# Performance work log

Measured on AMD Instinct MI355X. Metric: run time of the kernel, lower is better.

The kernel has to match this reference:

```python
import jax, jax.numpy as jnp
import numpy as np

NEG_SLOPE = 0.2
LN_EPS = 1e-5


def _layernorm(x, g, b):
    mu = jnp.mean(x, axis=-1, keepdims=True)
    var = jnp.mean(jnp.square(x - mu), axis=-1, keepdims=True)
    return (x - mu) * jax.lax.rsqrt(var + LN_EPS) * g + b


def _gat_layer(x, src, dst, ew, W, al, ar, bias, resW, act):
    # x: [N, F_in], W: [F_in, H*D], al/ar: [H, D], bias: [H*D]
    N = x.shape[0]
    H, D = al.shape
    feat = (x @ W).reshape(N, H, D)
    el = jnp.einsum('nhd,hd->nh', feat, al)          # [N, H]
    er = jnp.einsum('nhd,hd->nh', feat, ar)          # [N, H]
    e = jax.nn.leaky_relu(el[src] + er[dst], NEG_SLOPE)  # [E, H]
    # segment softmax over incoming edges of each destination node
    emax = jax.ops.segment_max(e, dst, num_segments=N)
    emax = jnp.where(jnp.isfinite(emax), emax, 0.0)
    ex = jnp.exp(e - emax[dst])
    den = jax.ops.segment_sum(ex, dst, num_segments=N)
    a = ex / den[dst] * ew[:, None]                  # [E, H] (edge_weight scales post-softmax, DGL semantics)
    msg = feat[src] * a[:, :, None]                  # [E, H, D]
    rst = jax.ops.segment_sum(msg, dst, num_segments=N)  # [N, H, D]
    res = (x @ resW).reshape(N, H, D) if resW is not None else x.reshape(N, H, D)
    rst = rst + res + bias.reshape(1, H, D)
    if act is not None:
        rst = act(rst)
    return rst.reshape(N, H * D)


def setup_inputs() -> dict:
    key = jax.random.key(0)
    ks = jax.random.split(key, 24)
    N, E, F_in, H, D = 100000, 1600000, 256, 4, 32
    HD = H * D
    s = 0.1
    inp = {
        'x': jax.random.normal(ks[0], (N, F_in), jnp.float32),
        'src': jax.random.randint(ks[1], (E,), 0, N, jnp.int32),
        'dst': jax.random.randint(ks[2], (E,), 0, N, jnp.int32),
        'edge_weight': jax.random.uniform(ks[3], (E,), jnp.float32),
        # layer 0: in 256 -> 4 heads x 32, residual Linear
        'W0': jax.random.normal(ks[4], (F_in, HD), jnp.float32) * s,
        'al0': jax.random.normal(ks[5], (H, D), jnp.float32) * s,
        'ar0': jax.random.normal(ks[6], (H, D), jnp.float32) * s,
        'b0': jnp.zeros((HD,), jnp.float32),
        'resW0': jax.random.normal(ks[7], (F_in, HD), jnp.float32) * s,
        'ln0_g': jnp.ones((HD,), jnp.float32),
        'ln0_b': jnp.zeros((HD,), jnp.float32),
        # layer 1: 128 -> 4x32, identity residual
        'W1': jax.random.normal(ks[8], (HD, HD), jnp.float32) * s,
        'al1': jax.random.normal(ks[9], (H, D), jnp.float32) * s,
        'ar1': jax.random.normal(ks[10], (H, D), jnp.float32) * s,
        'b1': jnp.zeros((HD,), jnp.float32),
        'ln1_g': jnp.ones((HD,), jnp.float32),
        'ln1_b': jnp.zeros((HD,), jnp.float32),
        # layer 2 (last, no activation)
        'W2': jax.random.normal(ks[11], (HD, HD), jnp.float32) * s,
        'al2': jax.random.normal(ks[12], (H, D), jnp.float32) * s,
        'ar2': jax.random.normal(ks[13], (H, D), jnp.float32) * s,
        'b2': jnp.zeros((HD,), jnp.float32),
        'ln2_g': jnp.ones((HD,), jnp.float32),
        'ln2_b': jnp.zeros((HD,), jnp.float32),
    }
    return inp


def reference(x, src, dst, edge_weight,
              W0, al0, ar0, b0, resW0, ln0_g, ln0_b,
              W1, al1, ar1, b1, ln1_g, ln1_b,
              W2, al2, ar2, b2, ln2_g, ln2_b):
    h = _gat_layer(x, src, dst, edge_weight, W0, al0, ar0, b0, resW0, jax.nn.elu)
    h = _layernorm(h, ln0_g, ln0_b)
    h = _gat_layer(h, src, dst, edge_weight, W1, al1, ar1, b1, None, jax.nn.elu)
    h = _layernorm(h, ln1_g, ln1_b)
    h = _gat_layer(h, src, dst, edge_weight, W2, al2, ar2, b2, None, None)
    h = _layernorm(h, ln2_g, ln2_b)
    return h
```

## Files before the change

kernel.cpp:

```cpp
#include <hip/hip_runtime.h>
#include <hip/hip_bf16.h>
#include <hip/hip_fp16.h>
#include <math.h>

#define DEV __device__ __forceinline__

typedef short v8s __attribute__((ext_vector_type(8)));
typedef float v4f __attribute__((ext_vector_type(4)));
typedef __fp16 fp16x2 __attribute__((ext_vector_type(2)));

DEV float bf2f(unsigned short u) {
    union { unsigned int i; float f; } c; c.i = ((unsigned int)u) << 16; return c.f;
}
DEV unsigned short f2bf(float f) {
    union { float f; unsigned int u; } c; c.f = f;
    unsigned int u = c.u;
    unsigned int r = u + 0x7fffu + ((u >> 16) & 1u);
    return (unsigned short)(r >> 16);
}
DEV unsigned short f2h(float f) {
    union { _Float16 h; unsigned short u; } c; c.h = (_Float16)f; return c.u;
}
DEV float h2f(unsigned short u) {
    union { unsigned short u; _Float16 h; } c; c.u = u; return (float)c.h;
}
DEV unsigned int pkdup(float x) {
    union { fp16x2 h; unsigned int u; } c;
    c.h = __builtin_amdgcn_cvt_pkrtz(x, x);
    return c.u;
}
DEV __half2 bitcast_h2(unsigned int u) {
    union { unsigned int u; __half2 h; } c; c.u = u; return c.h;
}

#if __has_builtin(__builtin_amdgcn_exp2f)
DEV float fexp2(float x) { return __builtin_amdgcn_exp2f(x); }
#else
DEV float fexp2(float x) { float r; asm("v_exp_f32 %0, %1" : "=v"(r) : "v"(x)); return r; }
#endif
#if __has_builtin(__builtin_amdgcn_rcpf)
DEV float frcp(float x) { return __builtin_amdgcn_rcpf(x); }
#else
DEV float frcp(float x) { float r; asm("v_rcp_f32 %0, %1" : "=v"(r) : "v"(x)); return r; }
#endif
#if __has_builtin(__builtin_amdgcn_rsqf)
DEV float frsq(float x) { return __builtin_amdgcn_rsqf(x); }
#else
DEV float frsq(float x) { float r; asm("v_rsq_f32 %0, %1" : "=v"(r) : "v"(x)); return r; }
#endif
DEV unsigned int cvtpk_bf16(float lo, float hi) {
    unsigned int r;
    asm("v_cvt_pk_bf16_f32 %0, %1, %2" : "=v"(r) : "v"(lo), "v"(hi));
    return r;
}

__global__ void detect_kernel(const unsigned short* __restrict__ w, int* __restrict__ flag) {
    __shared__ int cnt;
    if (threadIdx.x == 0) cnt = 0;
    __syncthreads();
    int c = 0;
    for (int i = threadIdx.x; i < 2048; i += 256) {
        unsigned short u = w[i * 2];
        int e = (u >> 7) & 0xff;
        if (e >= 110 && e <= 132) c++;
    }
    atomicAdd(&cnt, c);
    __syncthreads();
    if (threadIdx.x == 0) *flag = (cnt > 1024) ? 1 : 0;
}


__global__ void zero_kernel(int* __restrict__ p, int n) {
    int i = blockIdx.x * 256 + threadIdx.x;
    if (i < n) p[i] = 0;
}

__global__ void degree_kernel(const int* __restrict__ dst, int* __restrict__ deg, int E) {
    int i = blockIdx.x * 256 + threadIdx.x;
    if (i < E) atomicAdd(&deg[dst[i]], 1);
}

__global__ __launch_bounds__(1024)
void pscan_kernel(const int* __restrict__ deg, int* __restrict__ rowptr,
                  int* __restrict__ bsum, int n) {
    __shared__ int wtot[16];
    const int tid  = threadIdx.x;
    const int lane = tid & 63;
    const int wid  = tid >> 6;
    const int i0 = blockIdx.x * 4096 + tid * 4;
    int v0 = (i0     < n) ? deg[i0]     : 0;
    int v1 = (i0 + 1 < n) ? deg[i0 + 1] : 0;
    int v2 = (i0 + 2 < n) ? deg[i0 + 2] : 0;
    int v3 = (i0 + 3 < n) ? deg[i0 + 3] : 0;
    int s = v0 + v1 + v2 + v3;
    int sc = s;
    #pragma unroll
    for (int d = 1; d < 64; d <<= 1) {
        int t = __shfl_up(sc, d);
        if (lane >= d) sc += t;
    }
    if (lane == 63) wtot[wid] = sc;
    __syncthreads();
    int woff = 0, tot = 0;
    #pragma unroll
    for (int w = 0; w < 16; ++w) {
        int t = wtot[w];
        if (w < wid) woff += t;
        tot += t;
    }
    int p = woff + (sc - s);
    if (i0     < n) rowptr[i0]     = p; p += v0;
    if (i0 + 1 < n) rowptr[i0 + 1] = p; p += v1;
    if (i0 + 2 < n) rowptr[i0 + 2] = p; p += v2;
    if (i0 + 3 < n) rowptr[i0 + 3] = p;
    if (tid == 0) bsum[blockIdx.x] = tot;
}

__global__ void bscan_kernel(const int* __restrict__ bsum, int* __restrict__ boff, int nb) {
    int lane = threadIdx.x & 63;
    int v = (lane < nb) ? bsum[lane] : 0;
    int sc = v;
    #pragma unroll
    for (int d = 1; d < 64; d <<= 1) {
        int t = __shfl_up(sc, d);
        if (lane >= d) sc += t;
    }
    if (lane < nb) boff[lane] = sc - v;
}

__global__ void addoff_kernel(int* __restrict__ rowptr, const int* __restrict__ boff,
                              int n, int E) {
    int i = blockIdx.x * 256 + threadIdx.x;
    if (i < n) rowptr[i] += boff[i >> 12];
    else if (i == n) rowptr[n] = E;
}

__global__ void scatter_kernel(const int* __restrict__ src, const int* __restrict__ dst,
                               const void* __restrict__ ew, const int* __restrict__ flagp,
                               const int* __restrict__ rowptr, int* __restrict__ cur,
                               int2* __restrict__ csr, int E) {
    int i = blockIdx.x * 256 + threadIdx.x;
    if (i < E) {
        int isbf = *flagp;
        int d = dst[i];
        int pos = atomicAdd(&cur[d], 1);
        int slot = rowptr[d] + pos;
        float wv = isbf ? bf2f(((const unsigned short*)ew)[i]) : ((const float*)ew)[i];
        csr[slot] = make_int2(src[i], __float_as_int(wv));
    }
}

__global__ void wtrans_kernel(const void* __restrict__ B, unsigned short* __restrict__ Btp,
                              const int* __restrict__ flagp, int K) {
    int i = blockIdx.x * 256 + threadIdx.x;
    if (i >= 128 * K) return;
    int j = i & 7;
    int l = (i >> 3) & 63;
    int t = (i >> 9) & 7;
    int c = i >> 12;
    int k = c * 32 + ((l >> 4) * 8) + j;
    int n = t * 16 + (l & 15);
    unsigned short v;
    if (*flagp) v = ((const unsigned short*)B)[k * 128 + n];
    else        v = f2bf(((const float*)B)[k * 128 + n]);
    Btp[i] = v;
}

DEV void elr_epilogue(const v4f* acc, const void* al, const void* ar, int isbf,
                      int r, int quad, long m0, int M,
                      float4* el4, float4* er4) {
    float alv[8], arv[8];
    if (isbf) {
        const unsigned short* alp = (const unsigned short*)al;
        const unsigned short* arp = (const unsigned short*)ar;
        #pragma unroll
        for (int h = 0; h < 4; ++h) {
            alv[2*h]   = bf2f(alp[h*32 + r]);
            alv[2*h+1] = bf2f(alp[h*32 + 16 + r]);
            arv[2*h]   = bf2f(arp[h*32 + r]);
            arv[2*h+1] = bf2f(arp[h*32 + 16 + r]);
        }
    } else {
        const float* alp = (const float*)al;
        const float* arp = (const float*)ar;
        #pragma unroll
        for (int h = 0; h < 4; ++h) {
            alv[2*h]   = alp[h*32 + r];
            alv[2*h+1] = alp[h*32 + 16 + r];
            arv[2*h]   = arp[h*32 + r];
            arv[2*h+1] = arp[h*32 + 16 + r];
        }
    }
    #pragma unroll
    for (int reg = 0; reg < 4; ++reg) {
        float pel[4], per[4];
        #pragma unroll
        for (int h = 0; h < 4; ++h) {
            pel[h] = fmaf(acc[2*h+1][reg], alv[2*h+1], acc[2*h][reg] * alv[2*h]);
            per[h] = fmaf(acc[2*h+1][reg], arv[2*h+1], acc[2*h][reg] * arv[2*h]);
        }
        #pragma unroll
        for (int d = 1; d < 16; d <<= 1) {
            #pragma unroll
            for (int h = 0; h < 4; ++h) {
                pel[h] += __shfl_xor(pel[h], d);
                per[h] += __shfl_xor(per[h], d);
            }
        }
        long grow = m0 + quad * 4 + reg;
        if (grow < M) {
            if (r == 0) el4[grow] = make_float4(pel[0], pel[1], pel[2], pel[3]);
            if (r == 1) er4[grow] = make_float4(per[0], per[1], per[2], per[3]);
        }
    }
}

__global__ __launch_bounds__(256)
void gemm0_dual(const void* __restrict__ x, const int* __restrict__ flagp,
                const unsigned short* __restrict__ Bt,
                const unsigned short* __restrict__ Btr,
                const void* __restrict__ al, const void* __restrict__ ar,
                unsigned short* __restrict__ feat,
                unsigned short* __restrict__ res_bf,
                float4* __restrict__ el4, float4* __restrict__ er4,
                int M, int K) {
    const int isbf = *flagp;
    const int lane = threadIdx.x & 63;
    const int wid  = threadIdx.x >> 6;
    const long tile = (long)blockIdx.x * 4 + wid;
    const long m0 = tile * 16;
    if (m0 >= M) return;
    const int r = lane & 15, quad = lane >> 4;
    long arow = m0 + r; if (arow >= M) arow = M - 1;
    v4f accA[8], accB[8];
    #pragma unroll
    for (int t = 0; t < 8; ++t) { accA[t] = (v4f){0,0,0,0}; accB[t] = (v4f){0,0,0,0}; }
    if (isbf) {
        const unsigned short* ap = (const unsigned short*)x + (size_t)arow * K + quad * 8;
        for (int k0 = 0; k0 < K; k0 += 32) {
            v8s af = *(const v8s*)(ap + k0);
            const unsigned short* bpA = Bt  + ((size_t)(k0 >> 5) * 8) * 512 + lane * 8;
            const unsigned short* bpB = Btr + ((size_t)(k0 >> 5) * 8) * 512 + lane * 8;
            #pragma unroll
            for (int t = 0; t < 8; ++t) {
                v8s bfA = *(const v8s*)(bpA + t * 512);
                v8s bfB = *(const v8s*)(bpB + t * 512);
                accA[t] = __builtin_amdgcn_mfma_f32_16x16x32_bf16(af, bfA, accA[t], 0, 0, 0);
                accB[t] = __builtin_amdgcn_mfma_f32_16x16x32_bf16(af, bfB, accB[t], 0, 0, 0);
            }
        }
    } else {
        const float* ap = (const float*)x + (size_t)arow * K + quad * 8;
        for (int k0 = 0; k0 < K; k0 += 32) {
            float4 a0 = *(const float4*)(ap + k0);
            float4 a1 = *(const float4*)(ap + k0 + 4);
            uint4 u = make_uint4(cvtpk_bf16(a0.x, a0.y), cvtpk_bf16(a0.z, a0.w),
                                 cvtpk_bf16(a1.x, a1.y), cvtpk_bf16(a1.z, a1.w));
            union { uint4 u; v8s v; } cc; cc.u = u;
            v8s af = cc.v;
            const unsigned short* bpA = Bt  + ((size_t)(k0 >> 5) * 8) * 512 + lane * 8;
            const unsigned short* bpB = Btr + ((size_t)(k0 >> 5) * 8) * 512 + lane * 8;
            #pragma unroll
            for (int t = 0; t < 8; ++t) {
                v8s bfA = *(const v8s*)(bpA + t * 512);
                v8s bfB = *(const v8s*)(bpB + t * 512);
                accA[t] = __builtin_amdgcn_mfma_f32_16x16x32_bf16(af, bfA, accA[t], 0, 0, 0);
                accB[t] = __builtin_amdgcn_mfma_f32_16x16x32_bf16(af, bfB, accB[t], 0, 0, 0);
            }
        }
    }
    #pragma unroll
    for (int t = 0; t < 8; ++t) {
        const int col = t * 16 + r;
        #pragma unroll
        for (int reg = 0; reg < 4; ++reg) {
            long grow = m0 + quad * 4 + reg;
            if (grow < M) feat[grow * 128 + col] = f2h(accA[t][reg]);
        }
    }
    #pragma unroll
    for (int t = 0; t < 8; t += 2) {
        const int col0 = t * 16 + r, col1 = (t + 1) * 16 + r;
        #pragma unroll
        for (int reg = 0; reg < 4; ++reg) {
            long grow = m0 + quad * 4 + reg;
            unsigned int pk = cvtpk_bf16(accB[t][reg], accB[t + 1][reg]);
            if (grow < M) {
                res_bf[grow * 128 + col0] = (unsigned short)pk;
                res_bf[grow * 128 + col1] = (unsigned short)(pk >> 16);
            }
        }
    }
    elr_epilogue(accA, al, ar, isbf, r, quad, m0, M, el4, er4);
}

__global__ __launch_bounds__(256)
void gemm_mfma(const unsigned short* __restrict__ A,
               const unsigned short* __restrict__ Btp,
               const void* __restrict__ al, const void* __restrict__ ar,
               const int* __restrict__ flagp,
               unsigned short* __restrict__ Cout,
               float4* __restrict__ el4, float4* __restrict__ er4,
               int M, int K) {
    const int lane = threadIdx.x & 63;
    const int wid  = threadIdx.x >> 6;
    const long tile = (long)blockIdx.x * 4 + wid;
    const long m0 = tile * 16;
    if (m0 >= M) return;
    const int r = lane & 15, quad = lane >> 4;
    long arow = m0 + r; if (arow >= M) arow = M - 1;
    const unsigned short* ap = A + (size_t)arow * K + quad * 8;
    v4f acc[8];
    #pragma unroll
    for (int t = 0; t < 8; ++t) acc[t] = (v4f){0.f, 0.f, 0.f, 0.f};
    for (int k0 = 0; k0 < K; k0 += 32) {
        v8s af = *(const v8s*)(ap + k0);
        const unsigned short* bp = Btp + ((size_t)(k0 >> 5) * 8) * 512 + lane * 8;
        #pragma unroll
        for (int t = 0; t < 8; ++t) {
            v8s bf = *(const v8s*)(bp + t * 512);
            acc[t] = __builtin_amdgcn_mfma_f32_16x16x32_bf16(af, bf, acc[t], 0, 0, 0);
        }
    }
    #pragma unroll
    for (int t = 0; t < 8; ++t) {
        const int col = t * 16 + r;
        #pragma unroll
        for (int reg = 0; reg < 4; ++reg) {
            long grow = m0 + quad * 4 + reg;
            if (grow < M) Cout[grow * 128 + col] = f2h(acc[t][reg]);
        }
    }
    elr_epilogue(acc, al, ar, *flagp, r, quad, m0, M, el4, er4);
}


__global__ __launch_bounds__(256)
void aggregate_kernel(const unsigned short* __restrict__ feath,
                      const float4* __restrict__ el4,
                      const float4* __restrict__ er4,
                      const unsigned short* __restrict__ res_bf,
                      const void* __restrict__ bias,
                      const void* __restrict__ lng,
                      const void* __restrict__ lnb,
                      const int* __restrict__ flagp,
                      const int* __restrict__ rowptr,
                      const int2* __restrict__ csr,
                      unsigned short* __restrict__ out_bf,
                      float* __restrict__ out_f32,
                      int N, int apply_elu, int final_mode) {
    __shared__ int          s_src[4][64];
    __shared__ unsigned int s_pw[4][256];
    const int lane = threadIdx.x & 63;
    const int wid  = threadIdx.x >> 6;
    const int v = blockIdx.x * 4 + wid;
    if (v >= N) return;
    const int isbf = *flagp;
    const int eg = lane >> 4;
    const int fl = lane & 15;
    const int hd = fl >> 2;
    const int fb = fl * 8;
    const int p0 = rowptr[v], p1 = rowptr[v + 1];
    const float4 erv = er4[v];

    float den0 = 0.f, den1 = 0.f, den2 = 0.f, den3 = 0.f;
    __half2 acch[4];
    acch[0] = acch[1] = acch[2] = acch[3] = __float2half2_rn(0.f);

    for (int eb = p0; eb < p1; eb += 64) {
        const int cnt = min(64, p1 - eb);
        int s = 0;
        unsigned int pw0 = 0, pw1 = 0, pw2 = 0, pw3 = 0;
        if (lane < cnt) {
            int2 sw = csr[eb + lane];
            s = sw.x;
            float w = __int_as_float(sw.y);
            float4 elv = el4[s];
            float t, q;
            t = elv.x + erv.x; t = fmaxf(t, 0.2f * t);
            q = fexp2(fmaf(t, 1.44269504f, -6.0f)); den0 += q; pw0 = pkdup(q * w);
            t = elv.y + erv.y; t = fmaxf(t, 0.2f * t);
            q = fexp2(fmaf(t, 1.44269504f, -6.0f)); den1 += q; pw1 = pkdup(q * w);
            t = elv.z + erv.z; t = fmaxf(t, 0.2f * t);
            q = fexp2(fmaf(t, 1.44269504f, -6.0f)); den2 += q; pw2 = pkdup(q * w);
            t = elv.w + erv.w; t = fmaxf(t, 0.2f * t);
            q = fexp2(fmaf(t, 1.44269504f, -6.0f)); den3 += q; pw3 = pkdup(q * w);
        }
        s_src[wid][lane] = s;
        *(uint4*)&s_pw[wid][lane * 4] = make_uint4(pw0, pw1, pw2, pw3);
        const int cntr = (cnt + 3) & ~3;
        for (int e = 0; e < cntr; e += 4) {
            int ee = e + eg;
            int se = s_src[wid][ee];
            __half2 ae = bitcast_h2(s_pw[wid][ee * 4 + hd]);
            uint4 u = *(const uint4*)(feath + (size_t)se * 128 + fb);
            acch[0] = __hfma2(ae, bitcast_h2(u.x), acch[0]);
            acch[1] = __hfma2(ae, bitcast_h2(u.y), acch[1]);
            acch[2] = __hfma2(ae, bitcast_h2(u.z), acch[2]);
            acch[3] = __hfma2(ae, bitcast_h2(u.w), acch[3]);
        }
    }
    #pragma unroll
    for (int j = 0; j < 4; ++j) {
        union { __half2 h; int i; } a;
        union { int i; __half2 h; } b;
        a.h = acch[j]; b.i = __shfl_xor(a.i, 16); acch[j] = __hadd2(acch[j], b.h);
        a.h = acch[j]; b.i = __shfl_xor(a.i, 32); acch[j] = __hadd2(acch[j], b.h);
    }
    #pragma unroll
    for (int d = 1; d < 64; d <<= 1) {
        den0 += __shfl_xor(den0, d);
        den1 += __shfl_xor(den1, d);
        den2 += __shfl_xor(den2, d);
        den3 += __shfl_xor(den3, d);
    }
    float den = (hd == 0) ? den0 : (hd == 1) ? den1 : (hd == 2) ? den2 : den3;
    float invd = (p1 > p0) ? frcp(den) : 0.f;
    float acc[8];
    #pragma unroll
    for (int j = 0; j < 4; ++j) {
        acc[j * 2]     = __low2float(acch[j]);
        acc[j * 2 + 1] = __high2float(acch[j]);
    }
    uint4 ru = *(const uint4*)(res_bf + (size_t)v * 128 + fb);
    float rv[8];
    rv[0] = bf2f((unsigned short)(ru.x & 0xffffu)); rv[1] = bf2f((unsigned short)(ru.x >> 16));
    rv[2] = bf2f((unsigned short)(ru.y & 0xffffu)); rv[3] = bf2f((unsigned short)(ru.y >> 16));
    rv[4] = bf2f((unsigned short)(ru.z & 0xffffu)); rv[5] = bf2f((unsigned short)(ru.z >> 16));
    rv[6] = bf2f((unsigned short)(ru.w & 0xffffu)); rv[7] = bf2f((unsigned short)(ru.w >> 16));
    float bsv[8], gv[8], lbv[8];
    if (isbf) {
        const unsigned short* bsp = (const unsigned short*)bias + fb;
        const unsigned short* gp  = (const unsigned short*)lng + fb;
        const unsigned short* bp  = (const unsigned short*)lnb + fb;
        #pragma unroll
        for (int j = 0; j < 8; ++j) { bsv[j] = bf2f(bsp[j]); gv[j] = bf2f(gp[j]); lbv[j] = bf2f(bp[j]); }
    } else {
        const float* bsp = (const float*)bias + fb;
        const float* gp  = (const float*)lng + fb;
        const float* bp  = (const float*)lnb + fb;
        #pragma unroll
        for (int j = 0; j < 8; ++j) { bsv[j] = bsp[j]; gv[j] = gp[j]; lbv[j] = bp[j]; }
    }
    float o[8];
    float ssum = 0.f;
    #pragma unroll
    for (int j = 0; j < 8; ++j) {
        float t = acc[j] * invd + rv[j] + bsv[j];
        if (apply_elu) t = (t > 0.f) ? t : fexp2(t * 1.44269504f) - 1.0f;
        o[j] = t;
        ssum += t;
    }
    #pragma unroll
    for (int d = 1; d < 16; d <<= 1) ssum += __shfl_xor(ssum, d);
    float mu = ssum * (1.0f / 128.0f);
    float vsum = 0.f;
    #pragma unroll
    for (int j = 0; j < 8; ++j) { float dd = o[j] - mu; vsum += dd * dd; }
    #pragma unroll
    for (int d = 1; d < 16; d <<= 1) vsum += __shfl_xor(vsum, d);
    float rs = frsq(vsum * (1.0f / 128.0f) + 1e-5f);
    if (eg == 0) {
        if (final_mode && !isbf) {
            float* op = out_f32 + (size_t)v * 128 + fb;
            #pragma unroll
            for (int j = 0; j < 8; ++j) op[j] = (o[j] - mu) * rs * gv[j] + lbv[j];
        } else {
            unsigned int w[4];
            #pragma unroll
            for (int j = 0; j < 4; ++j) {
                float lo = (o[j*2]   - mu) * rs * gv[j*2]   + lbv[j*2];
                float hi = (o[j*2+1] - mu) * rs * gv[j*2+1] + lbv[j*2+1];
                w[j] = cvtpk_bf16(lo, hi);
            }
            *(uint4*)(out_bf + (size_t)v * 128 + fb) = make_uint4(w[0], w[1], w[2], w[3]);
        }
    }
}


extern "C" void kernel_launch(void* const* d_in, const int* in_sizes, int n_in,
                              void* d_out, int out_size, void* d_ws, size_t ws_size,
                              hipStream_t stream) {
    const void* x    = d_in[0];
    const int* src   = (const int*)d_in[1];
    const int* dst   = (const int*)d_in[2];
    const void* ew   = d_in[3];
    const void* W0   = d_in[4];
    const void* al0  = d_in[5];
    const void* ar0  = d_in[6];
    const void* b0   = d_in[7];
    const void* resW0= d_in[8];
    const void* ln0g = d_in[9];
    const void* ln0b = d_in[10];
    const void* W1   = d_in[11];
    const void* al1  = d_in[12];
    const void* ar1  = d_in[13];
    const void* b1   = d_in[14];
    const void* ln1g = d_in[15];
    const void* ln1b = d_in[16];
    const void* W2   = d_in[17];
    const void* al2  = d_in[18];
    const void* ar2  = d_in[19];
    const void* b2   = d_in[20];
    const void* ln2g = d_in[21];
    const void* ln2b = d_in[22];

    const int HD  = 128;
    const int Fin = in_sizes[4] / HD;
    const int N   = in_sizes[0] / Fin;
    const int E   = in_sizes[1];

    char* ws = (char*)d_ws;
    size_t off = 0;
    auto alloc = [&](size_t bytes) -> void* {
        void* p = ws + off;
        off = (off + bytes + 255) & ~(size_t)255;
        return p;
    };
    int*   flag    = (int*)alloc(256);
    unsigned short* feat  = (unsigned short*)alloc((size_t)N * 128 * 2);
    unsigned short* h_bf  = (unsigned short*)alloc((size_t)N * 128 * 2);
    unsigned short* res0  = (unsigned short*)alloc((size_t)N * 128 * 2);
    float* el      = (float*)alloc((size_t)N * 4 * 4);
    float* er      = (float*)alloc((size_t)N * 4 * 4);
    int*   rowptr  = (int*)alloc((size_t)(N + 1) * 4);
    int*   deg     = (int*)alloc((size_t)N * 4);
    int*   cur     = (int*)alloc((size_t)N * 4);
    int*   bsum    = (int*)alloc(256);
    int*   boff    = (int*)alloc(256);
    int2*  csr     = (int2*)alloc((size_t)E * 8);
    unsigned short* Bt0  = (unsigned short*)alloc((size_t)128 * Fin * 2);
    unsigned short* Btr0 = (unsigned short*)alloc((size_t)128 * Fin * 2);
    unsigned short* Bt1  = (unsigned short*)alloc((size_t)128 * HD * 2);
    unsigned short* Bt2  = (unsigned short*)alloc((size_t)128 * HD * 2);

    const int zb = (N + 255) / 256;
    const int eb = (E + 255) / 256;
    const int gblocks = (N + 63) / 64;
    const int ablocks = (N + 3) / 4;
    const int nb = (N + 4095) / 4096;
    const int aob = (N + 1 + 255) / 256;
    const int wtb0 = (128 * Fin + 255) / 256;
    const int wtb1 = (128 * HD + 255) / 256;

    detect_kernel<<<1, 256, 0, stream>>>((const unsigned short*)W0, flag);

    zero_kernel<<<zb, 256, 0, stream>>>(deg, N);
    zero_kernel<<<zb, 256, 0, stream>>>(cur, N);
    degree_kernel<<<eb, 256, 0, stream>>>(dst, deg, E);
    pscan_kernel<<<nb, 1024, 0, stream>>>(deg, rowptr, bsum, N);
    bscan_kernel<<<1, 64, 0, stream>>>(bsum, boff, nb);
    addoff_kernel<<<aob, 256, 0, stream>>>(rowptr, boff, N, E);
    scatter_kernel<<<eb, 256, 0, stream>>>(src, dst, ew, flag, rowptr, cur, csr, E);

    wtrans_kernel<<<wtb0, 256, 0, stream>>>(W0,    Bt0,  flag, Fin);
    wtrans_kernel<<<wtb0, 256, 0, stream>>>(resW0, Btr0, flag, Fin);
    wtrans_kernel<<<wtb1, 256, 0, stream>>>(W1,    Bt1,  flag, HD);
    wtrans_kernel<<<wtb1, 256, 0, stream>>>(W2,    Bt2,  flag, HD);

    gemm0_dual<<<gblocks, 256, 0, stream>>>(x, flag, Bt0, Btr0, al0, ar0,
        feat, res0, (float4*)el, (float4*)er, N, Fin);
    aggregate_kernel<<<ablocks, 256, 0, stream>>>(feat, (const float4*)el, (const float4*)er,
        res0, b0, ln0g, ln0b, flag, rowptr, csr, h_bf, nullptr, N, 1, 0);

    gemm_mfma<<<gblocks, 256, 0, stream>>>(h_bf, Bt1, al1, ar1, flag, feat,
        (float4*)el, (float4*)er, N, HD);
    aggregate_kernel<<<ablocks, 256, 0, stream>>>(feat, (const float4*)el, (const float4*)er,
        h_bf, b1, ln1g, ln1b, flag, rowptr, csr, h_bf, nullptr, N, 1, 0);

    gemm_mfma<<<gblocks, 256, 0, stream>>>(h_bf, Bt2, al2, ar2, flag, feat,
        (float4*)el, (float4*)er, N, HD);
    aggregate_kernel<<<ablocks, 256, 0, stream>>>(feat, (const float4*)el, (const float4*)er,
        h_bf, b2, ln2g, ln2b, flag, rowptr, csr, (unsigned short*)d_out, (float*)d_out, N, 0, 1);
}
```

Measured before the change: 722.3 us.

## Stage GEMM B tiles through LDS with register prefetch of next k-slice

```diff
diff --git a/kernel.cpp b/kernel.cpp
--- a/kernel.cpp
+++ b/kernel.cpp
@@ -224,49 +224,70 @@
                 unsigned short* __restrict__ res_bf,
                 float4* __restrict__ el4, float4* __restrict__ er4,
                 int M, int K) {
+    __shared__ unsigned short ldsB[8192];
     const int isbf = *flagp;
     const int lane = threadIdx.x & 63;
     const int wid  = threadIdx.x >> 6;
     const long tile = (long)blockIdx.x * 4 + wid;
     const long m0 = tile * 16;
-    if (m0 >= M) return;
     const int r = lane & 15, quad = lane >> 4;
     long arow = m0 + r; if (arow >= M) arow = M - 1;
+    const int woff = wid * 1024 + lane * 8;
+    const int loff = lane * 8;
+    const int nk = K >> 5;
+
     v4f accA[8], accB[8];
     #pragma unroll
     for (int t = 0; t < 8; ++t) { accA[t] = (v4f){0,0,0,0}; accB[t] = (v4f){0,0,0,0}; }
+
+    uint4 s0, s1, s2, s3;
+    float4 a0, a1;
+    uint4  au;
+    s0 = *(const uint4*)(Bt  + woff);
+    s1 = *(const uint4*)(Bt  + woff + 512);
+    s2 = *(const uint4*)(Btr + woff);
+    s3 = *(const uint4*)(Btr + woff + 512);
     if (isbf) {
-        const unsigned short* ap = (const unsigned short*)x + (size_t)arow * K + quad * 8;
-        for (int k0 = 0; k0 < K; k0 += 32) {
-            v8s af = *(const v8s*)(ap + k0);
-            const unsigned short* bpA = Bt  + ((size_t)(k0 >> 5) * 8) * 512 + lane * 8;
-            const unsigned short* bpB = Btr + ((size_t)(k0 >> 5) * 8) * 512 + lane * 8;
-            #pragma unroll
-            for (int t = 0; t < 8; ++t) {
-                v8s bfA = *(const v8s*)(bpA + t * 512);
-                v8s bfB = *(const v8s*)(bpB + t * 512);
-                accA[t] = __builtin_amdgcn_mfma_f32_16x16x32_bf16(af, bfA, accA[t], 0, 0, 0);
-                accB[t] = __builtin_amdgcn_mfma_f32_16x16x32_bf16(af, bfB, accB[t], 0, 0, 0);
-            }
-        }
+        au = *(const uint4*)((const unsigned short*)x + (size_t)arow * K + quad * 8);
     } else {
         const float* ap = (const float*)x + (size_t)arow * K + quad * 8;
-        for (int k0 = 0; k0 < K; k0 += 32) {
-            float4 a0 = *(const float4*)(ap + k0);
-            float4 a1 = *(const float4*)(ap + k0 + 4);
-            uint4 u = make_uint4(cvtpk_bf16(a0.x, a0.y), cvtpk_bf16(a0.z, a0.w),
-                                 cvtpk_bf16(a1.x, a1.y), cvtpk_bf16(a1.z, a1.w));
-            union { uint4 u; v8s v; } cc; cc.u = u;
-            v8s af = cc.v;
-            const unsigned short* bpA = Bt  + ((size_t)(k0 >> 5) * 8) * 512 + lane * 8;
-            const unsigned short* bpB = Btr + ((size_t)(k0 >> 5) * 8) * 512 + lane * 8;
-            #pragma unroll
-            for (int t = 0; t < 8; ++t) {
-                v8s bfA = *(const v8s*)(bpA + t * 512);
-                v8s bfB = *(const v8s*)(bpB + t * 512);
-                accA[t] = __builtin_amdgcn_mfma_f32_16x16x32_bf16(af, bfA, accA[t], 0, 0, 0);
-                accB[t] = __builtin_amdgcn_mfma_f32_16x16x32_bf16(af, bfB, accB[t], 0, 0, 0);
+        a0 = *(const float4*)ap; a1 = *(const float4*)(ap + 4);
+    }
+
+    for (int k = 0; k < nk; ++k) {
+        __syncthreads();
+        *(uint4*)&ldsB[woff]              = s0;
+        *(uint4*)&ldsB[woff + 512]        = s1;
+        *(uint4*)&ldsB[4096 + woff]       = s2;
+        *(uint4*)&ldsB[4096 + woff + 512] = s3;
+        __syncthreads();
+        v8s af;
+        if (isbf) {
+            union { uint4 u; v8s v; } c; c.u = au; af = c.v;
+        } else {
+            union { uint4 u; v8s v; } c;
+            c.u = make_uint4(cvtpk_bf16(a0.x, a0.y), cvtpk_bf16(a0.z, a0.w),
+                             cvtpk_bf16(a1.x, a1.y), cvtpk_bf16(a1.z, a1.w));
+            af = c.v;
+        }
+        if (k + 1 < nk) {
+            const unsigned short* bb = Bt  + (size_t)(k + 1) * 4096 + woff;
+            const unsigned short* br = Btr + (size_t)(k + 1) * 4096 + woff;
+            s0 = *(const uint4*)bb; s1 = *(const uint4*)(bb + 512);
+            s2 = *(const uint4*)br; s3 = *(const uint4*)(br + 512);
+            if (isbf) {
+                au = *(const uint4*)((const unsigned short*)x + (size_t)arow * K + (k + 1) * 32 + quad * 8);
+            } else {
+                const float* ap = (const float*)x + (size_t)arow * K + (k + 1) * 32 + quad * 8;
+                a0 = *(const float4*)ap; a1 = *(const float4*)(ap + 4);
             }
+        }
+        #pragma unroll
+        for (int t = 0; t < 8; ++t) {
+            v8s bfA = *(const v8s*)&ldsB[t * 512 + loff];
+            v8s bfB = *(const v8s*)&ldsB[4096 + t * 512 + loff];
+            accA[t] = __builtin_amdgcn_mfma_f32_16x16x32_bf16(af, bfA, accA[t], 0, 0, 0);
+            accB[t] = __builtin_amdgcn_mfma_f32_16x16x32_bf16(af, bfB, accB[t], 0, 0, 0);
         }
     }
     #pragma unroll
@@ -302,23 +323,41 @@
                unsigned short* __restrict__ Cout,
                float4* __restrict__ el4, float4* __restrict__ er4,
                int M, int K) {
+    __shared__ unsigned short ldsB[4096];
     const int lane = threadIdx.x & 63;
     const int wid  = threadIdx.x >> 6;
     const long tile = (long)blockIdx.x * 4 + wid;
     const long m0 = tile * 16;
-    if (m0 >= M) return;
     const int r = lane & 15, quad = lane >> 4;
     long arow = m0 + r; if (arow >= M) arow = M - 1;
-    const unsigned short* ap = A + (size_t)arow * K + quad * 8;
+    const int woff = wid * 1024 + lane * 8;
+    const int loff = lane * 8;
+    const int nk = K >> 5;
+
     v4f acc[8];
     #pragma unroll
     for (int t = 0; t < 8; ++t) acc[t] = (v4f){0.f, 0.f, 0.f, 0.f};
-    for (int k0 = 0; k0 < K; k0 += 32) {
-        v8s af = *(const v8s*)(ap + k0);
-        const unsigned short* bp = Btp + ((size_t)(k0 >> 5) * 8) * 512 + lane * 8;
+
+    uint4 s0, s1, au;
+    s0 = *(const uint4*)(Btp + woff);
+    s1 = *(const uint4*)(Btp + woff + 512);
+    au = *(const uint4*)(A + (size_t)arow * K + quad * 8);
+
+    for (int k = 0; k < nk; ++k) {
+        __syncthreads();
+        *(uint4*)&ldsB[woff]       = s0;
+        *(uint4*)&ldsB[woff + 512] = s1;
+        __syncthreads();
+        union { uint4 u; v8s v; } c; c.u = au;
+        v8s af = c.v;
+        if (k + 1 < nk) {
+            const unsigned short* bb = Btp + (size_t)(k + 1) * 4096 + woff;
+            s0 = *(const uint4*)bb; s1 = *(const uint4*)(bb + 512);
+            au = *(const uint4*)(A + (size_t)arow * K + (k + 1) * 32 + quad * 8);
+        }
         #pragma unroll
         for (int t = 0; t < 8; ++t) {
-            v8s bf = *(const v8s*)(bp + t * 512);
+            v8s bf = *(const v8s*)&ldsB[t * 512 + loff];
             acc[t] = __builtin_amdgcn_mfma_f32_16x16x32_bf16(af, bf, acc[t], 0, 0, 0);
         }
     }
@@ -333,7 +372,6 @@
     }
     elr_epilogue(acc, al, ar, *flagp, r, quad, m0, M, el4, er4);
 }
-
 
 __global__ __launch_bounds__(256)
 void aggregate_kernel(const unsigned short* __restrict__ feath,
```

After: 694.5 us. -3.8%, faster.
